# Kernel optimization log

Hardware: AMD Instinct MI355X
Metric: run time of the kernel (lower is better)

## Reference

```python
import jax, jax.numpy as jnp
import numpy as np

VOCAB, EMB, HID, LAYERS, SEQ, BATCH = 10000, 1024, 1024, 2, 64, 64


def setup_inputs() -> dict:
    key = jax.random.key(0)
    ks = jax.random.split(key, 12)
    b = 1.0 / np.sqrt(HID)
    u = lambda k, shape, bd: jax.random.uniform(k, shape, jnp.float32, -bd, bd)
    return {
        "inputs": jax.random.randint(ks[0], (SEQ, BATCH), 0, VOCAB),
        "hidden": jnp.zeros((LAYERS, BATCH, HID), jnp.float32),
        "emb": u(ks[1], (VOCAB, EMB), 0.1),
        "W0": u(ks[2], (EMB, 3 * HID), b),
        "U0": u(ks[3], (HID, 3 * HID), b),
        "bw0": u(ks[4], (3 * HID,), b),
        "bu0": u(ks[5], (3 * HID,), b),
        "W1": u(ks[6], (HID, 3 * HID), b),
        "U1": u(ks[7], (HID, 3 * HID), b),
        "bw1": u(ks[8], (3 * HID,), b),
        "bu1": u(ks[9], (3 * HID,), b),
        "fcW": u(ks[10], (VOCAB, HID), 0.1),
        "fcb": jnp.zeros((VOCAB,), jnp.float32),
    }


def gru_cell(x, h, W, U, bw, bu):
    gx = x @ W + bw            # [B, 3H]
    gh = h @ U + bu            # [B, 3H]
    i_r, i_z, i_n = jnp.split(gx, 3, axis=1)
    h_r, h_z, h_n = jnp.split(gh, 3, axis=1)
    r = jax.nn.sigmoid(i_r + h_r)
    z = jax.nn.sigmoid(i_z + h_z)
    h_tilde = jnp.tanh(i_n + r * h_n)
    return (1.0 - z) * h + z * h_tilde


def reference(inputs, hidden, emb, W0, U0, bw0, bu0, W1, U1, bw1, bu1, fcW, fcb):
    # dp_keep_prob = 1.0 -> dropout is identity (eval-mode reference)
    def step(hid, tok):
        x = emb[tok]                                   # [B, EMB]
        h0 = gru_cell(x, hid[0], W0, U0, bw0, bu0)     # [B, H]
        h1 = gru_cell(h0, hid[1], W1, U1, bw1, bu1)    # [B, H]
        y = h1 @ fcW.T + fcb                           # [B, V]
        return jnp.stack([h0, h1]), y

    hidden_f, logits = jax.lax.scan(step, hidden, inputs)
    return logits, hidden_f
```

## Files before the change

kernel.cpp:

```cpp
#include <hip/hip_runtime.h>
#include <math.h>

#define SEQL 64
#define BATCHN 64
#define HID 1024
#define EMBD 1024
#define VOCAB 10000
#define G3 3072
#define NPAD 10240
#define AROWS 4096
#define HSLOT 65536

typedef float f4v __attribute__((ext_vector_type(4)));
typedef unsigned short us4 __attribute__((ext_vector_type(4)));
typedef unsigned short us8 __attribute__((ext_vector_type(8)));
typedef __bf16 bf8v __attribute__((ext_vector_type(8)));

__device__ __forceinline__ unsigned short f2bf(float f) {
    unsigned u = __float_as_uint(f);
    u += 0x7fffu + ((u >> 16) & 1u);
    return (unsigned short)(u >> 16);
}
__device__ __forceinline__ float bf2f(unsigned short h) {
    return __uint_as_float(((unsigned)h) << 16);
}
__device__ __forceinline__ void split2(float f, unsigned short &hi, unsigned short &lo) {
    hi = f2bf(f);
    lo = f2bf(f - bf2f(hi));
}
__device__ __forceinline__ f4v mfma16(us8 a, us8 b, f4v c) {
    return __builtin_amdgcn_mfma_f32_16x16x32_bf16(
        __builtin_bit_cast(bf8v, a), __builtin_bit_cast(bf8v, b), c, 0, 0, 0);
}
__device__ __forceinline__ float sigmoidf_(float x) { return 1.f / (1.f + expf(-x)); }

__device__ __forceinline__ size_t htile_off(int b, int j) {
    return ((size_t)((((b >> 4) * 32 + (j >> 5)) * 64) + ((j >> 3) & 3) * 16 + (b & 15))) * 8 + (j & 7);
}

__global__ __launch_bounds__(256)
void tile_weights_kernel(const float* __restrict__ U0, const float* __restrict__ W1,
                         const float* __restrict__ U1, const float* __restrict__ W0,
                         unsigned short* __restrict__ hi, unsigned short* __restrict__ lo)
{
    __shared__ float tile[32][65];
    const int mat = blockIdx.z;
    const float* src = (mat == 0) ? U0 : (mat == 1) ? W1 : (mat == 2) ? U1 : W0;
    const int n0 = blockIdx.x * 64, k0 = blockIdx.y * 32;
    const int t = threadIdx.x, tx = t & 63, ty = t >> 6;
#pragma unroll
    for (int s = 0; s < 8; s++)
        tile[ty * 8 + s][tx] = src[(size_t)(k0 + ty * 8 + s) * G3 + n0 + tx];
    __syncthreads();
    const int c = t >> 6, lane = t & 63, fr = lane & 15, kg = lane >> 4;
    const int cc = (n0 >> 4) + c;
    const size_t off = (((size_t)(mat * 192 + cc) * 32 + (k0 >> 5)) * 64 + lane) * 8;
    us8 h8, l8;
#pragma unroll
    for (int e = 0; e < 8; e++) {
        unsigned short a, b;
        split2(tile[kg * 8 + e][c * 16 + fr], a, b);
        h8[e] = a; l8[e] = b;
    }
    *(us8*)(hi + off) = h8;
    *(us8*)(lo + off) = l8;
}

__global__ void fc_pad_split_kernel(const float* __restrict__ fcW,
                                    unsigned short* __restrict__ hi, unsigned short* __restrict__ lo)
{
    size_t i = ((size_t)blockIdx.x * 256 + threadIdx.x) * 4;
    size_t row = i >> 10;
    f4v v = {0.f, 0.f, 0.f, 0.f};
    if (row < VOCAB) v = *(const f4v*)(fcW + i);
    us4 h, l;
#pragma unroll
    for (int j = 0; j < 4; j++) { unsigned short a, b; split2(v[j], a, b); h[j] = a; l[j] = b; }
    *(us4*)(hi + i) = h;
    *(us4*)(lo + i) = l;
}

__global__ void fcb_pad_kernel(const float* __restrict__ fcb, float* __restrict__ fcb_pad)
{
    int idx = blockIdx.x * 256 + threadIdx.x;
    if (idx < NPAD) fcb_pad[idx] = (idx < VOCAB) ? fcb[idx] : 0.f;
}

__global__ void small_prep_kernel(const float* __restrict__ hidden,
                                  unsigned short* __restrict__ h0th, unsigned short* __restrict__ h0tl,
                                  unsigned short* __restrict__ h1th, unsigned short* __restrict__ h1tl)
{
    int idx = blockIdx.x * 256 + threadIdx.x;
    if (idx < BATCHN * HID) {
        int b = idx >> 10, j = idx & 1023;
        size_t o = htile_off(b, j);
        unsigned short a1, b1;
        split2(hidden[idx], a1, b1);                 h0th[o] = a1; h0tl[o] = b1;
        split2(hidden[BATCHN * HID + idx], a1, b1);  h1th[o] = a1; h1tl[o] = b1;
    }
}

__global__ __launch_bounds__(256)
void gx0_gemm_kernel(const int* __restrict__ tok, const float* __restrict__ emb,
                     const unsigned short* __restrict__ Wthi, const unsigned short* __restrict__ Wtlo,
                     float* __restrict__ C)
{
    __shared__ unsigned short Ah[128][40], Al[128][40];
    const int bswz = blockIdx.x;
    const int xcd = bswz & 7, s = bswz >> 3;
    const int col0 = (xcd + 8 * (s >> 5)) * 128;
    const int row0 = (s & 31) * 128;
    const int tid = threadIdx.x;
    const int lane = tid & 63, wave = tid >> 6;
    const int wm = wave >> 1, wn = wave & 1;
    const int srow = tid >> 1;
    const int shalf = (tid & 1) * 16;

    const float* asrc = emb + (size_t)tok[row0 + srow] * EMBD + shalf;
    const int fr = lane & 15, fk = (lane >> 4) * 8;
    const int cc0 = (col0 >> 4) + wn * 4;

    f4v a[4];
#pragma unroll
    for (int q = 0; q < 4; q++) a[q] = *(const f4v*)(asrc + q * 4);

    f4v acc[4][4] = {};
    for (int k0 = 0; k0 < EMBD; k0 += 32) {
        __syncthreads();
        us8 ahv[2], alv[2];
#pragma unroll
        for (int q = 0; q < 4; q++)
#pragma unroll
            for (int j = 0; j < 4; j++) {
                unsigned short h, l;
                split2(a[q][j], h, l);
                ahv[q >> 1][(q & 1) * 4 + j] = h;
                alv[q >> 1][(q & 1) * 4 + j] = l;
            }
        *(us8*)(&Ah[srow][shalf]) = ahv[0];     *(us8*)(&Ah[srow][shalf + 8]) = ahv[1];
        *(us8*)(&Al[srow][shalf]) = alv[0];     *(us8*)(&Al[srow][shalf + 8]) = alv[1];
        __syncthreads();
        if (k0 + 32 < EMBD) {
#pragma unroll
            for (int q = 0; q < 4; q++) a[q] = *(const f4v*)(asrc + k0 + 32 + q * 4);
        }
        const int ks = k0 >> 5;
        us8 bfh[4], bfl[4];
#pragma unroll
        for (int n = 0; n < 4; n++) {
            const size_t bo = (((size_t)(3 * 192 + cc0 + n) * 32 + ks) * 64 + lane) * 8;
            bfh[n] = *(const us8*)(Wthi + bo);
            bfl[n] = *(const us8*)(Wtlo + bo);
        }
        us8 afh[4], afl[4];
#pragma unroll
        for (int m = 0; m < 4; m++) {
            afh[m] = *(const us8*)(&Ah[wm * 64 + m * 16 + fr][fk]);
            afl[m] = *(const us8*)(&Al[wm * 64 + m * 16 + fr][fk]);
        }
#pragma unroll
        for (int n = 0; n < 4; n++)
#pragma unroll
            for (int m = 0; m < 4; m++) {
                acc[m][n] = mfma16(afh[m], bfh[n], acc[m][n]);
                acc[m][n] = mfma16(afh[m], bfl[n], acc[m][n]);
                acc[m][n] = mfma16(afl[m], bfh[n], acc[m][n]);
            }
    }
    const int fq = lane >> 4;
#pragma unroll
    for (int m = 0; m < 4; m++)
#pragma unroll
        for (int n = 0; n < 4; n++)
#pragma unroll
            for (int i = 0; i < 4; i++) {
                int r = row0 + wm * 64 + m * 16 + fq * 4 + i;
                int c = col0 + wn * 64 + n * 16 + fr;
                C[(size_t)r * G3 + c] = acc[m][n][i];
            }
}

__global__ __launch_bounds__(256)
void logits_gemm_kernel(const unsigned short* __restrict__ h1t_hi, const unsigned short* __restrict__ h1t_lo,
                        const unsigned short* __restrict__ Bhi, const unsigned short* __restrict__ Blo,
                        const float* __restrict__ bias, float* __restrict__ C)
{
    __shared__ unsigned short Bh[128][40], Bl[128][40];
    const int bswz = blockIdx.x;
    const int xcd = bswz & 7, s = bswz >> 3;
    const int col0 = (xcd + 8 * (s >> 5)) * 128;
    const int row0 = (s & 31) * 128;
    const int t0 = row0 >> 6;
    const int tid = threadIdx.x;
    const int lane = tid & 63, wave = tid >> 6;
    const int wm = wave >> 1, wn = wave & 1;
    const int srow = tid >> 1;
    const int shalf = (tid & 1) * 16;

    const unsigned short* bh_src = Bhi + (size_t)(col0 + srow) * HID + shalf;
    const unsigned short* bl_src = Blo + (size_t)(col0 + srow) * HID + shalf;

    f4v acc[4][4] = {};
    us8 bh2[2], bl2[2];
    bh2[0] = *(const us8*)(bh_src);  bh2[1] = *(const us8*)(bh_src + 8);
    bl2[0] = *(const us8*)(bl_src);  bl2[1] = *(const us8*)(bl_src + 8);

    const int fr = lane & 15, fk = (lane >> 4) * 8;
    const size_t abase = ((size_t)(t0 + wm) * 128) * 512 + (size_t)lane * 8;

    for (int k0 = 0; k0 < HID; k0 += 32) {
        __syncthreads();
        *(us8*)(&Bh[srow][shalf]) = bh2[0];  *(us8*)(&Bh[srow][shalf + 8]) = bh2[1];
        *(us8*)(&Bl[srow][shalf]) = bl2[0];  *(us8*)(&Bl[srow][shalf + 8]) = bl2[1];
        __syncthreads();
        if (k0 + 32 < HID) {
            bh2[0] = *(const us8*)(bh_src + k0 + 32);  bh2[1] = *(const us8*)(bh_src + k0 + 40);
            bl2[0] = *(const us8*)(bl_src + k0 + 32);  bl2[1] = *(const us8*)(bl_src + k0 + 40);
        }
        const int ks = k0 >> 5;
        us8 afh[4], afl[4];
#pragma unroll
        for (int m = 0; m < 4; m++) {
            const size_t ao = abase + (size_t)(m * 32 + ks) * 512;
            afh[m] = *(const us8*)(h1t_hi + ao);
            afl[m] = *(const us8*)(h1t_lo + ao);
        }
#pragma unroll
        for (int n = 0; n < 4; n++) {
            us8 bfh = *(const us8*)(&Bh[wn * 64 + n * 16 + fr][fk]);
            us8 bfl = *(const us8*)(&Bl[wn * 64 + n * 16 + fr][fk]);
#pragma unroll
            for (int m = 0; m < 4; m++) {
                acc[m][n] = mfma16(afh[m], bfh, acc[m][n]);
                acc[m][n] = mfma16(afh[m], bfl, acc[m][n]);
                acc[m][n] = mfma16(afl[m], bfh, acc[m][n]);
            }
        }
    }
    const int fq = lane >> 4;
#pragma unroll
    for (int m = 0; m < 4; m++)
#pragma unroll
        for (int n = 0; n < 4; n++)
#pragma unroll
            for (int i = 0; i < 4; i++) {
                int r = row0 + wm * 64 + m * 16 + fq * 4 + i;
                int c = col0 + wn * 64 + n * 16 + fr;
                float v = acc[m][n][i] + bias[c];
                if (c < VOCAB) C[(size_t)r * VOCAB + c] = v;
            }
}

template <int T0, int T1>
__global__ __launch_bounds__(512)
void step_gemm_kernel(const unsigned short* __restrict__ h0hi, const unsigned short* __restrict__ h0lo,
                      const unsigned short* __restrict__ h1hi, const unsigned short* __restrict__ h1lo,
                      const unsigned short* __restrict__ Wthi, const unsigned short* __restrict__ Wtlo,
                      float* __restrict__ P)
{
    __shared__ float red[4][9][16][17];
    const int tid = threadIdx.x, lane = tid & 63, wave = tid >> 6;
    const int wr = wave & 3, kh = wave >> 2;
    const int jc = blockIdx.x >> 2, kq = blockIdx.x & 3;

    f4v acc[9] = {};
#pragma unroll
    for (int ksl = 0; ksl < 4; ksl++) {
        const int ks = kq * 8 + kh * 4 + ksl;
        const size_t aoff = ((size_t)(wr * 32 + ks) * 64 + lane) * 8;
        us8 a0h = *(const us8*)(h0hi + aoff);
        us8 a0l = *(const us8*)(h0lo + aoff);
        us8 a1h = {}, a1l = {};
        if (T1 > 3) { a1h = *(const us8*)(h1hi + aoff); a1l = *(const us8*)(h1lo + aoff); }
#pragma unroll
        for (int g = 0; g < 3; g++) {
            const size_t base = (((size_t)(g * 64 + jc) * 32 + ks) * 64 + lane) * 8;
            if (T0 == 0) {
                us8 bh = *(const us8*)(Wthi + base);
                us8 bl = *(const us8*)(Wtlo + base);
                acc[g] = mfma16(a0h, bh, acc[g]);
                acc[g] = mfma16(a0h, bl, acc[g]);
                acc[g] = mfma16(a0l, bh, acc[g]);
            }
            if (T1 > 3) {
                const size_t b1 = base + (size_t)192 * 32 * 64 * 8;
                us8 bh = *(const us8*)(Wthi + b1);
                us8 bl = *(const us8*)(Wtlo + b1);
                acc[3 + g] = mfma16(a0h, bh, acc[3 + g]);
                acc[3 + g] = mfma16(a0h, bl, acc[3 + g]);
                acc[3 + g] = mfma16(a0l, bh, acc[3 + g]);
                const size_t b2 = base + (size_t)2 * 192 * 32 * 64 * 8;
                us8 ch = *(const us8*)(Wthi + b2);
                us8 cl = *(const us8*)(Wtlo + b2);
                acc[6 + g] = mfma16(a1h, ch, acc[6 + g]);
                acc[6 + g] = mfma16(a1h, cl, acc[6 + g]);
                acc[6 + g] = mfma16(a1l, ch, acc[6 + g]);
            }
        }
    }
    const int rrow = (lane >> 4) * 4, rcol = lane & 15;
    if (kh == 1) {
#pragma unroll
        for (int t2 = T0; t2 < T1; t2++)
#pragma unroll
            for (int i = 0; i < 4; i++) red[wr][t2][rrow + i][rcol] = acc[t2][i];
    }
    __syncthreads();
    if (kh == 0) {
#pragma unroll
        for (int t2 = T0; t2 < T1; t2++)
#pragma unroll
            for (int i = 0; i < 4; i++) {
                float v = acc[t2][i] + red[wr][t2][rrow + i][rcol];
                const int b = wr * 16 + rrow + i;
                P[(((size_t)kq * 9 + t2) * 64 + b) * 1024 + jc * 16 + rcol] = v;
            }
    }
}

template <int T0, int T1>
__global__ __launch_bounds__(256)
void step_reduce_kernel(const float* __restrict__ P, const float* __restrict__ gx0next,
                        const float* __restrict__ bw0, const float* __restrict__ bu0,
                        const float* __restrict__ bw1, const float* __restrict__ bu1,
                        const unsigned short* __restrict__ h0hi, const unsigned short* __restrict__ h0lo,
                        const unsigned short* __restrict__ h1hi, const unsigned short* __restrict__ h1lo,
                        unsigned short* __restrict__ h0o_hi, unsigned short* __restrict__ h0o_lo,
                        unsigned short* __restrict__ h1o_hi, unsigned short* __restrict__ h1o_lo)
{
    const int idx = blockIdx.x * 256 + threadIdx.x;
    const int b = idx >> 10, j = idx & 1023;
    float G[9];
#pragma unroll
    for (int t2 = T0; t2 < T1; t2++) {
        const float* p = P + ((size_t)t2 * 64 + b) * 1024 + j;
        G[t2] = (p[0] + p[(size_t)9 * 64 * 1024])
              + (p[(size_t)18 * 64 * 1024] + p[(size_t)27 * 64 * 1024]);
    }
    const size_t po = htile_off(b, j);
    if (T0 == 0) {
        float sr  = gx0next[(size_t)b * G3 + j]            + bw0[j]           + G[0] + bu0[j];
        float sz  = gx0next[(size_t)b * G3 + HID + j]      + bw0[HID + j]     + G[1] + bu0[HID + j];
        float gxn = gx0next[(size_t)b * G3 + 2 * HID + j]  + bw0[2 * HID + j];
        float ghn = G[2] + bu0[2 * HID + j];
        float r = sigmoidf_(sr);
        float z = sigmoidf_(sz);
        float ht = tanhf(gxn + r * ghn);
        float hp = bf2f(h0hi[po]) + bf2f(h0lo[po]);
        float hn = (1.f - z) * hp + z * ht;
        unsigned short hh, hl2; split2(hn, hh, hl2);
        h0o_hi[po] = hh; h0o_lo[po] = hl2;
    }
    if (T1 > 3) {
        float sr  = G[3] + bw1[j]           + G[6] + bu1[j];
        float sz  = G[4] + bw1[HID + j]     + G[7] + bu1[HID + j];
        float gxn = G[5] + bw1[2 * HID + j];
        float ghn = G[8] + bu1[2 * HID + j];
        float r = sigmoidf_(sr);
        float z = sigmoidf_(sz);
        float ht = tanhf(gxn + r * ghn);
        float hp = bf2f(h1hi[po]) + bf2f(h1lo[po]);
        float hn = (1.f - z) * hp + z * ht;
        unsigned short hh, hl2; split2(hn, hh, hl2);
        h1o_hi[po] = hh; h1o_lo[po] = hl2;
    }
}

__global__ void hidden_out_kernel(const unsigned short* __restrict__ h0hi, const unsigned short* __restrict__ h0lo,
                                  const unsigned short* __restrict__ h1hi, const unsigned short* __restrict__ h1lo,
                                  float* __restrict__ out)
{
    int i = blockIdx.x * 256 + threadIdx.x;
    if (i < BATCHN * HID) {
        int b = i >> 10, j = i & 1023;
        size_t o = htile_off(b, j);
        out[i] = bf2f(h0hi[o]) + bf2f(h0lo[o]);
        out[BATCHN * HID + i] = bf2f(h1hi[o]) + bf2f(h1lo[o]);
    }
}

extern "C" void kernel_launch(void* const* d_in, const int* in_sizes, int n_in,
                              void* d_out, int out_size, void* d_ws, size_t ws_size,
                              hipStream_t stream)
{
    (void)in_sizes; (void)n_in; (void)out_size;
    const int*   tok    = (const int*)  d_in[0];
    const float* hidden = (const float*)d_in[1];
    const float* emb    = (const float*)d_in[2];
    const float* W0     = (const float*)d_in[3];
    const float* U0     = (const float*)d_in[4];
    const float* bw0    = (const float*)d_in[5];
    const float* bu0    = (const float*)d_in[6];
    const float* W1     = (const float*)d_in[7];
    const float* U1     = (const float*)d_in[8];
    const float* bw1    = (const float*)d_in[9];
    const float* bu1    = (const float*)d_in[10];
    const float* fcW    = (const float*)d_in[11];
    const float* fcb    = (const float*)d_in[12];
    float* out = (float*)d_out;

    char* wsp = (char*)d_ws;
    size_t used = 0;
    auto alloc = [&](size_t bytes) -> char* {
        char* p = wsp + used;
        used += (bytes + 255) & ~(size_t)255;
        return p;
    };
    unsigned short* Wt_hi = (unsigned short*)alloc((size_t)4 * G3 * HID * 2);
    unsigned short* Wt_lo = (unsigned short*)alloc((size_t)4 * G3 * HID * 2);
    float*          GX0   = (float*)alloc((size_t)AROWS * G3 * 4);
    unsigned short* H0Thi = (unsigned short*)alloc((size_t)SEQL * HSLOT * 2);
    unsigned short* H0Tlo = (unsigned short*)alloc((size_t)SEQL * HSLOT * 2);
    unsigned short* H1Thi = (unsigned short*)alloc((size_t)SEQL * HSLOT * 2);
    unsigned short* H1Tlo = (unsigned short*)alloc((size_t)SEQL * HSLOT * 2);
    float*          P0    = (float*)alloc((size_t)4 * 9 * BATCHN * HID * 4);
    float*          P1    = (float*)alloc((size_t)4 * 9 * BATCHN * HID * 4);
    unsigned short* h0ith = (unsigned short*)alloc((size_t)HSLOT * 2);
    unsigned short* h0itl = (unsigned short*)alloc((size_t)HSLOT * 2);
    unsigned short* h1ith = (unsigned short*)alloc((size_t)HSLOT * 2);
    unsigned short* h1itl = (unsigned short*)alloc((size_t)HSLOT * 2);
    if (used > ws_size) return;

    unsigned short* fcWhi = Wt_hi;
    unsigned short* fcWlo = Wt_lo;
    float*          fcbp  = (float*)((char*)Wt_hi + (size_t)NPAD * HID * 2);

    tile_weights_kernel<<<dim3(48, 32, 4), 256, 0, stream>>>(U0, W1, U1, W0, Wt_hi, Wt_lo);
    small_prep_kernel<<<256, 256, 0, stream>>>(hidden, h0ith, h0itl, h1ith, h1itl);
    gx0_gemm_kernel<<<768, 256, 0, stream>>>(tok, emb, Wt_hi, Wt_lo, GX0);

    step_gemm_kernel<0, 3><<<256, 512, 0, stream>>>(
        h0ith, h0itl, h1ith, h1itl, Wt_hi, Wt_lo, P0);
    step_reduce_kernel<0, 3><<<256, 256, 0, stream>>>(
        P0, GX0, bw0, bu0, bw1, bu1,
        h0ith, h0itl, h1ith, h1itl,
        H0Thi, H0Tlo,
        H1Thi + (size_t)63 * HSLOT, H1Tlo + (size_t)63 * HSLOT);

    for (int t = 0; t < 63; t++) {
        const unsigned short* h0h = H0Thi + (size_t)t * HSLOT;
        const unsigned short* h0l = H0Tlo + (size_t)t * HSLOT;
        const unsigned short* a1h = (t == 0) ? h1ith : H1Thi + (size_t)(t - 1) * HSLOT;
        const unsigned short* a1l = (t == 0) ? h1itl : H1Tlo + (size_t)(t - 1) * HSLOT;
        float* Pb = ((t & 1) == 0) ? P1 : P0;
        step_gemm_kernel<0, 9><<<256, 512, 0, stream>>>(
            h0h, h0l, a1h, a1l, Wt_hi, Wt_lo, Pb);
        step_reduce_kernel<0, 9><<<256, 256, 0, stream>>>(
            Pb, GX0 + (size_t)(t + 1) * BATCHN * G3, bw0, bu0, bw1, bu1,
            h0h, h0l, a1h, a1l,
            H0Thi + (size_t)(t + 1) * HSLOT, H0Tlo + (size_t)(t + 1) * HSLOT,
            H1Thi + (size_t)t * HSLOT, H1Tlo + (size_t)t * HSLOT);
    }
    step_gemm_kernel<3, 9><<<256, 512, 0, stream>>>(
        H0Thi + (size_t)63 * HSLOT, H0Tlo + (size_t)63 * HSLOT,
        H1Thi + (size_t)62 * HSLOT, H1Tlo + (size_t)62 * HSLOT,
        Wt_hi, Wt_lo, P0);
    step_reduce_kernel<3, 9><<<256, 256, 0, stream>>>(
        P0, GX0, bw0, bu0, bw1, bu1,
        H0Thi + (size_t)63 * HSLOT, H0Tlo + (size_t)63 * HSLOT,
        H1Thi + (size_t)62 * HSLOT, H1Tlo + (size_t)62 * HSLOT,
        h0ith, h0itl,
        H1Thi + (size_t)63 * HSLOT, H1Tlo + (size_t)63 * HSLOT);

    hidden_out_kernel<<<256, 256, 0, stream>>>(
        H0Thi + (size_t)63 * HSLOT, H0Tlo + (size_t)63 * HSLOT,
        H1Thi + (size_t)63 * HSLOT, H1Tlo + (size_t)63 * HSLOT,
        out + (size_t)AROWS * VOCAB);

    fc_pad_split_kernel<<<NPAD, 256, 0, stream>>>(fcW, fcWhi, fcWlo);
    fcb_pad_kernel<<<(NPAD + 255) / 256, 256, 0, stream>>>(fcb, fcbp);
    logits_gemm_kernel<<<2560, 256, 0, stream>>>(
        H1Thi, H1Tlo, fcWhi, fcWlo, fcbp, out);
}
```

Baseline: 1.695 ms.

## Fuse step GEMM and GRU reduction via last-block atomic counter

```diff
diff --git a/kernel.cpp b/kernel.cpp
--- a/kernel.cpp
+++ b/kernel.cpp
@@ -88,9 +88,11 @@
 
 __global__ void small_prep_kernel(const float* __restrict__ hidden,
                                   unsigned short* __restrict__ h0th, unsigned short* __restrict__ h0tl,
-                                  unsigned short* __restrict__ h1th, unsigned short* __restrict__ h1tl)
+                                  unsigned short* __restrict__ h1th, unsigned short* __restrict__ h1tl,
+                                  int* __restrict__ cnt)
 {
     int idx = blockIdx.x * 256 + threadIdx.x;
+    if (idx < 65 * 64) cnt[idx] = 0;
     if (idx < BATCHN * HID) {
         int b = idx >> 10, j = idx & 1023;
         size_t o = htile_off(b, j);
@@ -252,117 +254,143 @@
 }
 
 template <int T0, int T1>
-__global__ __launch_bounds__(512)
-void step_gemm_kernel(const unsigned short* __restrict__ h0hi, const unsigned short* __restrict__ h0lo,
-                      const unsigned short* __restrict__ h1hi, const unsigned short* __restrict__ h1lo,
-                      const unsigned short* __restrict__ Wthi, const unsigned short* __restrict__ Wtlo,
-                      float* __restrict__ P)
-{
-    __shared__ float red[4][9][16][17];
+__global__ __launch_bounds__(512, 2)
+void step_fused_kernel(const unsigned short* __restrict__ h0hi, const unsigned short* __restrict__ h0lo,
+                       const unsigned short* __restrict__ h1hi, const unsigned short* __restrict__ h1lo,
+                       const unsigned short* __restrict__ Wthi, const unsigned short* __restrict__ Wtlo,
+                       const float* __restrict__ gx0next,
+                       const float* __restrict__ bw0, const float* __restrict__ bu0,
+                       const float* __restrict__ bw1, const float* __restrict__ bu1,
+                       float* __restrict__ P, int* __restrict__ cntRow,
+                       unsigned short* __restrict__ h0o_hi, unsigned short* __restrict__ h0o_lo,
+                       unsigned short* __restrict__ h1o_hi, unsigned short* __restrict__ h1o_lo)
+{
     const int tid = threadIdx.x, lane = tid & 63, wave = tid >> 6;
-    const int wr = wave & 3, kh = wave >> 2;
     const int jc = blockIdx.x >> 2, kq = blockIdx.x & 3;
-
-    f4v acc[9] = {};
-#pragma unroll
-    for (int ksl = 0; ksl < 4; ksl++) {
-        const int ks = kq * 8 + kh * 4 + ksl;
-        const size_t aoff = ((size_t)(wr * 32 + ks) * 64 + lane) * 8;
-        us8 a0h = *(const us8*)(h0hi + aoff);
-        us8 a0l = *(const us8*)(h0lo + aoff);
-        us8 a1h = {}, a1l = {};
-        if (T1 > 3) { a1h = *(const us8*)(h1hi + aoff); a1l = *(const us8*)(h1lo + aoff); }
-#pragma unroll
-        for (int g = 0; g < 3; g++) {
-            const size_t base = (((size_t)(g * 64 + jc) * 32 + ks) * 64 + lane) * 8;
-            if (T0 == 0) {
-                us8 bh = *(const us8*)(Wthi + base);
-                us8 bl = *(const us8*)(Wtlo + base);
-                acc[g] = mfma16(a0h, bh, acc[g]);
-                acc[g] = mfma16(a0h, bl, acc[g]);
-                acc[g] = mfma16(a0l, bh, acc[g]);
-            }
-            if (T1 > 3) {
-                const size_t b1 = base + (size_t)192 * 32 * 64 * 8;
-                us8 bh = *(const us8*)(Wthi + b1);
-                us8 bl = *(const us8*)(Wtlo + b1);
-                acc[3 + g] = mfma16(a0h, bh, acc[3 + g]);
-                acc[3 + g] = mfma16(a0h, bl, acc[3 + g]);
-                acc[3 + g] = mfma16(a0l, bh, acc[3 + g]);
-                const size_t b2 = base + (size_t)2 * 192 * 32 * 64 * 8;
-                us8 ch = *(const us8*)(Wthi + b2);
-                us8 cl = *(const us8*)(Wtlo + b2);
-                acc[6 + g] = mfma16(a1h, ch, acc[6 + g]);
-                acc[6 + g] = mfma16(a1h, cl, acc[6 + g]);
-                acc[6 + g] = mfma16(a1l, ch, acc[6 + g]);
-            }
-        }
-    }
-    const int rrow = (lane >> 4) * 4, rcol = lane & 15;
-    if (kh == 1) {
-#pragma unroll
-        for (int t2 = T0; t2 < T1; t2++)
-#pragma unroll
-            for (int i = 0; i < 4; i++) red[wr][t2][rrow + i][rcol] = acc[t2][i];
-    }
+    const int ks = kq * 8 + wave;
+    const size_t abase = ((size_t)ks * 64 + lane) * 8;
+
+    us8 a0h[4], a0l[4], a1h[4], a1l[4];
+#pragma unroll
+    for (int m = 0; m < 4; m++) {
+        a0h[m] = *(const us8*)(h0hi + abase + (size_t)m * 16384);
+        a0l[m] = *(const us8*)(h0lo + abase + (size_t)m * 16384);
+    }
+    if (T1 > 3) {
+#pragma unroll
+        for (int m = 0; m < 4; m++) {
+            a1h[m] = *(const us8*)(h1hi + abase + (size_t)m * 16384);
+            a1l[m] = *(const us8*)(h1lo + abase + (size_t)m * 16384);
+        }
+    }
+
+    f4v acc[9][4] = {};
+#pragma unroll
+    for (int t2 = T0; t2 < T1; ++t2) {
+        const int mat = t2 / 3, g = t2 % 3;
+        const size_t base = (((size_t)(mat * 192 + g * 64 + jc) * 32 + ks) * 64 + lane) * 8;
+        us8 bh = *(const us8*)(Wthi + base);
+        us8 bl = *(const us8*)(Wtlo + base);
+#pragma unroll
+        for (int m = 0; m < 4; ++m) {
+            us8 ah = (t2 < 6) ? a0h[m] : a1h[m];
+            us8 al = (t2 < 6) ? a0l[m] : a1l[m];
+            acc[t2][m] = mfma16(ah, bh, acc[t2][m]);
+            acc[t2][m] = mfma16(ah, bl, acc[t2][m]);
+            acc[t2][m] = mfma16(al, bh, acc[t2][m]);
+        }
+    }
+
+    __shared__ f4v red[4][3][4][64];
+    const int c0lo = T0 / 3, c0hi = (T1 + 2) / 3;
+#pragma unroll
+    for (int stride = 4; stride >= 1; stride >>= 1) {
+#pragma unroll
+        for (int c = c0lo; c < c0hi; ++c) {
+            if (wave >= stride && wave < 2 * stride) {
+#pragma unroll
+                for (int u = 0; u < 3; ++u) {
+                    const int t2 = c * 3 + u;
+                    if (t2 >= T0 && t2 < T1) {
+#pragma unroll
+                        for (int m = 0; m < 4; ++m)
+                            red[wave - stride][u][m][lane] = acc[t2][m];
+                    }
+                }
+            }
+            __syncthreads();
+            if (wave < stride) {
+#pragma unroll
+                for (int u = 0; u < 3; ++u) {
+                    const int t2 = c * 3 + u;
+                    if (t2 >= T0 && t2 < T1) {
+#pragma unroll
+                        for (int m = 0; m < 4; ++m)
+                            acc[t2][m] += red[wave][u][m][lane];
+                    }
+                }
+            }
+            __syncthreads();
+        }
+    }
+
+    if (wave == 0) {
+        const int rrow = (lane >> 4) * 4, rcol = lane & 15;
+#pragma unroll
+        for (int t2 = T0; t2 < T1; ++t2)
+#pragma unroll
+            for (int m = 0; m < 4; ++m)
+#pragma unroll
+                for (int i = 0; i < 4; ++i)
+                    P[(((size_t)kq * 9 + t2) * 64 + (m * 16 + rrow + i)) * 1024 + jc * 16 + rcol]
+                        = acc[t2][m][i];
+    }
+    __threadfence();
     __syncthreads();
-    if (kh == 0) {
-#pragma unroll
-        for (int t2 = T0; t2 < T1; t2++)
-#pragma unroll
-            for (int i = 0; i < 4; i++) {
-                float v = acc[t2][i] + red[wr][t2][rrow + i][rcol];
-                const int b = wr * 16 + rrow + i;
-                P[(((size_t)kq * 9 + t2) * 64 + b) * 1024 + jc * 16 + rcol] = v;
-            }
-    }
-}
-
-template <int T0, int T1>
-__global__ __launch_bounds__(256)
-void step_reduce_kernel(const float* __restrict__ P, const float* __restrict__ gx0next,
-                        const float* __restrict__ bw0, const float* __restrict__ bu0,
-                        const float* __restrict__ bw1, const float* __restrict__ bu1,
-                        const unsigned short* __restrict__ h0hi, const unsigned short* __restrict__ h0lo,
-                        const unsigned short* __restrict__ h1hi, const unsigned short* __restrict__ h1lo,
-                        unsigned short* __restrict__ h0o_hi, unsigned short* __restrict__ h0o_lo,
-                        unsigned short* __restrict__ h1o_hi, unsigned short* __restrict__ h1o_lo)
-{
-    const int idx = blockIdx.x * 256 + threadIdx.x;
-    const int b = idx >> 10, j = idx & 1023;
-    float G[9];
-#pragma unroll
-    for (int t2 = T0; t2 < T1; t2++) {
-        const float* p = P + ((size_t)t2 * 64 + b) * 1024 + j;
-        G[t2] = (p[0] + p[(size_t)9 * 64 * 1024])
-              + (p[(size_t)18 * 64 * 1024] + p[(size_t)27 * 64 * 1024]);
-    }
-    const size_t po = htile_off(b, j);
-    if (T0 == 0) {
-        float sr  = gx0next[(size_t)b * G3 + j]            + bw0[j]           + G[0] + bu0[j];
-        float sz  = gx0next[(size_t)b * G3 + HID + j]      + bw0[HID + j]     + G[1] + bu0[HID + j];
-        float gxn = gx0next[(size_t)b * G3 + 2 * HID + j]  + bw0[2 * HID + j];
-        float ghn = G[2] + bu0[2 * HID + j];
-        float r = sigmoidf_(sr);
-        float z = sigmoidf_(sz);
-        float ht = tanhf(gxn + r * ghn);
-        float hp = bf2f(h0hi[po]) + bf2f(h0lo[po]);
-        float hn = (1.f - z) * hp + z * ht;
-        unsigned short hh, hl2; split2(hn, hh, hl2);
-        h0o_hi[po] = hh; h0o_lo[po] = hl2;
-    }
-    if (T1 > 3) {
-        float sr  = G[3] + bw1[j]           + G[6] + bu1[j];
-        float sz  = G[4] + bw1[HID + j]     + G[7] + bu1[HID + j];
-        float gxn = G[5] + bw1[2 * HID + j];
-        float ghn = G[8] + bu1[2 * HID + j];
-        float r = sigmoidf_(sr);
-        float z = sigmoidf_(sz);
-        float ht = tanhf(gxn + r * ghn);
-        float hp = bf2f(h1hi[po]) + bf2f(h1lo[po]);
-        float hn = (1.f - z) * hp + z * ht;
-        unsigned short hh, hl2; split2(hn, hh, hl2);
-        h1o_hi[po] = hh; h1o_lo[po] = hl2;
+    __shared__ int lastFlag;
+    if (tid == 0) lastFlag = (atomicAdd(cntRow + jc, 1) == 3);
+    __syncthreads();
+    if (!lastFlag) return;
+    __threadfence();
+
+#pragma unroll
+    for (int k = 0; k < 2; ++k) {
+        const int idx = k * 512 + tid;
+        const int b = idx >> 4, j = jc * 16 + (idx & 15);
+        float G[9] = {};
+#pragma unroll
+        for (int t2 = T0; t2 < T1; ++t2) {
+            const float* p = P + ((size_t)t2 * 64 + b) * 1024 + j;
+            G[t2] = (p[0] + p[(size_t)9 * 64 * 1024])
+                  + (p[(size_t)18 * 64 * 1024] + p[(size_t)27 * 64 * 1024]);
+        }
+        const size_t po = htile_off(b, j);
+        if (T0 == 0) {
+            float sr  = gx0next[(size_t)b * G3 + j]            + bw0[j]           + G[0] + bu0[j];
+            float sz  = gx0next[(size_t)b * G3 + HID + j]      + bw0[HID + j]     + G[1] + bu0[HID + j];
+            float gxn = gx0next[(size_t)b * G3 + 2 * HID + j]  + bw0[2 * HID + j];
+            float ghn = G[2] + bu0[2 * HID + j];
+            float r = sigmoidf_(sr);
+            float z = sigmoidf_(sz);
+            float ht = tanhf(gxn + r * ghn);
+            float hp = bf2f(h0hi[po]) + bf2f(h0lo[po]);
+            float hn = (1.f - z) * hp + z * ht;
+            unsigned short hh, hl2; split2(hn, hh, hl2);
+            h0o_hi[po] = hh; h0o_lo[po] = hl2;
+        }
+        if (T1 > 3) {
+            float sr  = G[3] + bw1[j]           + G[6] + bu1[j];
+            float sz  = G[4] + bw1[HID + j]     + G[7] + bu1[HID + j];
+            float gxn = G[5] + bw1[2 * HID + j];
+            float ghn = G[8] + bu1[2 * HID + j];
+            float r = sigmoidf_(sr);
+            float z = sigmoidf_(sz);
+            float ht = tanhf(gxn + r * ghn);
+            float hp = bf2f(h1hi[po]) + bf2f(h1lo[po]);
+            float hn = (1.f - z) * hp + z * ht;
+            unsigned short hh, hl2; split2(hn, hh, hl2);
+            h1o_hi[po] = hh; h1o_lo[po] = hl2;
+        }
     }
 }
 
@@ -415,6 +443,7 @@
     unsigned short* H1Tlo = (unsigned short*)alloc((size_t)SEQL * HSLOT * 2);
     float*          P0    = (float*)alloc((size_t)4 * 9 * BATCHN * HID * 4);
     float*          P1    = (float*)alloc((size_t)4 * 9 * BATCHN * HID * 4);
+    int*            cnt   = (int*)alloc((size_t)65 * 64 * 4);
     unsigned short* h0ith = (unsigned short*)alloc((size_t)HSLOT * 2);
     unsigned short* h0itl = (unsigned short*)alloc((size_t)HSLOT * 2);
     unsigned short* h1ith = (unsigned short*)alloc((size_t)HSLOT * 2);
@@ -426,14 +455,12 @@
     float*          fcbp  = (float*)((char*)Wt_hi + (size_t)NPAD * HID * 2);
 
     tile_weights_kernel<<<dim3(48, 32, 4), 256, 0, stream>>>(U0, W1, U1, W0, Wt_hi, Wt_lo);
-    small_prep_kernel<<<256, 256, 0, stream>>>(hidden, h0ith, h0itl, h1ith, h1itl);
+    small_prep_kernel<<<256, 256, 0, stream>>>(hidden, h0ith, h0itl, h1ith, h1itl, cnt);
     gx0_gemm_kernel<<<768, 256, 0, stream>>>(tok, emb, Wt_hi, Wt_lo, GX0);
 
-    step_gemm_kernel<0, 3><<<256, 512, 0, stream>>>(
-        h0ith, h0itl, h1ith, h1itl, Wt_hi, Wt_lo, P0);
-    step_reduce_kernel<0, 3><<<256, 256, 0, stream>>>(
-        P0, GX0, bw0, bu0, bw1, bu1,
-        h0ith, h0itl, h1ith, h1itl,
+    step_fused_kernel<0, 3><<<256, 512, 0, stream>>>(
+        h0ith, h0itl, h1ith, h1itl, Wt_hi, Wt_lo,
+        GX0, bw0, bu0, bw1, bu1, P0, cnt,
         H0Thi, H0Tlo,
         H1Thi + (size_t)63 * HSLOT, H1Tlo + (size_t)63 * HSLOT);
 
@@ -443,22 +470,18 @@
         const unsigned short* a1h = (t == 0) ? h1ith : H1Thi + (size_t)(t - 1) * HSLOT;
         const unsigned short* a1l = (t == 0) ? h1itl : H1Tlo + (size_t)(t - 1) * HSLOT;
         float* Pb = ((t & 1) == 0) ? P1 : P0;
-        step_gemm_kernel<0, 9><<<256, 512, 0, stream>>>(
-            h0h, h0l, a1h, a1l, Wt_hi, Wt_lo, Pb);
-        step_reduce_kernel<0, 9><<<256, 256, 0, stream>>>(
-            Pb, GX0 + (size_t)(t + 1) * BATCHN * G3, bw0, bu0, bw1, bu1,
-            h0h, h0l, a1h, a1l,
+        step_fused_kernel<0, 9><<<256, 512, 0, stream>>>(
+            h0h, h0l, a1h, a1l, Wt_hi, Wt_lo,
+            GX0 + (size_t)(t + 1) * BATCHN * G3, bw0, bu0, bw1, bu1,
+            Pb, cnt + (size_t)(t + 1) * 64,
             H0Thi + (size_t)(t + 1) * HSLOT, H0Tlo + (size_t)(t + 1) * HSLOT,
             H1Thi + (size_t)t * HSLOT, H1Tlo + (size_t)t * HSLOT);
     }
-    step_gemm_kernel<3, 9><<<256, 512, 0, stream>>>(
+    step_fused_kernel<3, 9><<<256, 512, 0, stream>>>(
         H0Thi + (size_t)63 * HSLOT, H0Tlo + (size_t)63 * HSLOT,
         H1Thi + (size_t)62 * HSLOT, H1Tlo + (size_t)62 * HSLOT,
-        Wt_hi, Wt_lo, P0);
-    step_reduce_kernel<3, 9><<<256, 256, 0, stream>>>(
-        P0, GX0, bw0, bu0, bw1, bu1,
-        H0Thi + (size_t)63 * HSLOT, H0Tlo + (size_t)63 * HSLOT,
-        H1Thi + (size_t)62 * HSLOT, H1Tlo + (size_t)62 * HSLOT,
+        Wt_hi, Wt_lo,
+        GX0, bw0, bu0, bw1, bu1, P0, cnt + (size_t)64 * 64,
         h0ith, h0itl,
         H1Thi + (size_t)63 * HSLOT, H1Tlo + (size_t)63 * HSLOT);
 
```

After: 5.729 ms. 238% more time.
